# Performance work log

Measured on AMD Instinct MI355X. Metric: run time of the kernel, lower is better.

## Reference

```python
import jax, jax.numpy as jnp
import numpy as np

B, C, HW, N, FS = 8, 1024, 14, 512, 14  # batch, channels, fmap size, num ROIs, feature_scal
SCALE = 1.0 / 16.0
IMG = 224.0


def setup_inputs() -> dict:
    key = jax.random.key(0)
    k1, k2, k3, k4 = jax.random.split(key, 4)
    tensor = jax.random.normal(k1, (B, C, HW, HW), dtype=jnp.float32)
    # ROI rows: [batch_idx, x1, y1, x2, y2] in 224-px image coords, guaranteed x2>x1, y2>y1
    bidx = jax.random.randint(k2, (N,), 0, B).astype(jnp.float32)
    xy1 = jax.random.uniform(k3, (N, 2), minval=0.0, maxval=100.0)
    wh = jax.random.uniform(k4, (N, 2), minval=16.0, maxval=124.0)
    xy2 = jnp.minimum(xy1 + wh, IMG)
    ROI = jnp.concatenate([bidx[:, None], xy1, xy2], axis=1)  # [N,5]
    return {"tensor": tensor, "ROI": ROI}


def _pool_matrix(start, end, fs):
    # Adaptive-avg-pool of slice [start:end] (length L) to fs bins, expressed as a
    # [N, fs(out bins), fs(input positions)] averaging matrix.
    L = end - start  # [N] ints, >= 1
    i = jnp.arange(fs)  # output bins
    b0 = (i[None, :] * L[:, None]) // fs                      # [N,fs] bin start (rel)
    b1 = ((i[None, :] + 1) * L[:, None] + fs - 1) // fs       # [N,fs] bin end (rel, excl)
    pos = jnp.arange(fs)[None, None, :] - start[:, None, None]  # [N,1,fs] rel input pos
    mask = (pos >= b0[:, :, None]) & (pos < b1[:, :, None])     # [N,fs,fs]
    cnt = jnp.maximum(b1 - b0, 1).astype(jnp.float32)
    return mask.astype(jnp.float32) / cnt[:, :, None]


def reference(tensor, ROI):
    fm_no = ROI[:, 0].astype(jnp.int32)          # which batch element per ROI
    coords = ROI[:, 1:] * SCALE                  # [N,4] = x1,y1,x2,y2 in fmap coords
    x1 = jnp.maximum(jnp.floor(coords[:, 0]), 0).astype(jnp.int32)
    y1 = jnp.maximum(jnp.floor(coords[:, 1]), 0).astype(jnp.int32)
    x2 = jnp.minimum(jnp.ceil(coords[:, 2]), FS).astype(jnp.int32)
    y2 = jnp.minimum(jnp.ceil(coords[:, 3]), FS).astype(jnp.int32)
    # torch code slices fm[:, :, x1:x2, y1:y2] -> x indexes rows (H), y indexes cols (W)
    Mr = _pool_matrix(x1, x2, FS)  # [N,14,14] row pooling
    Mc = _pool_matrix(y1, y2, FS)  # [N,14,14] col pooling
    fms = tensor[fm_no]            # [N,C,14,14] gather per-ROI feature map
    # pooled[n,c,i,j] = sum_{h,w} Mr[n,i,h] * fms[n,c,h,w] * Mc[n,j,w]
    return jnp.einsum('nih,nchw,njw->ncij', Mr, fms, Mc)
```

## Files before the change

### kernel.cpp

```cpp
#include <hip/hip_runtime.h>


#define FS_      14
#define PER_CH   196
#define C_       1024
#define CPB      32
#define QPC      49
#define NSTAGE4  (CPB * PER_CH / 4)
#define ACT      245

#if defined(__has_builtin)
# if __has_builtin(__builtin_amdgcn_global_load_lds)
#  define USE_GLL 1
# endif
#endif

__global__ __launch_bounds__(256) void roi_pool_kernel(
    const float* __restrict__ tensor,
    const float* __restrict__ roi,
    float* __restrict__ out)
{
    __shared__ float s_plane[CPB * PER_CH + 4];
    __shared__ alignas(16) int   s_o00[PER_CH], s_o10[PER_CH];
    __shared__ alignas(16) float s_mw[PER_CH], s_mh[PER_CH], s_inv[PER_CH];

    const unsigned bx = blockIdx.x;
    const unsigned n  = bx >> 5;
    const unsigned c0 = (bx & 31u) * CPB;

    const float* r = roi + n * 5;
    const int fm = (int)r[0];
    const int x1 = max((int)floorf(r[1] * 0.0625f), 0);
    const int y1 = max((int)floorf(r[2] * 0.0625f), 0);
    const int x2 = min((int)ceilf(r[3] * 0.0625f), FS_);
    const int y2 = min((int)ceilf(r[4] * 0.0625f), FS_);
    const unsigned Lh = (unsigned)(x2 - x1);
    const unsigned Lw = (unsigned)(y2 - y1);

    const unsigned tid = threadIdx.x;

    if (tid < PER_CH) {
        const unsigned p = tid;
        const unsigned i = p / 14u;
        const unsigned j = p - i * 14u;
        const unsigned h0 = (i * Lh) / 14u;
        const unsigned h1 = ((i + 1u) * Lh + 13u) / 14u;
        const unsigned w0 = (j * Lw) / 14u;
        const unsigned w1 = ((j + 1u) * Lw + 13u) / 14u;
        const int dh = (int)(h1 - h0) - 1;
        const int dw = (int)(w1 - w0) - 1;
        const int a00 = (x1 + (int)h0) * FS_ + (y1 + (int)w0);
        s_o00[p] = a00 * 4;
        s_o10[p] = (a00 + FS_ * dh) * 4;
        s_mw[p]  = (float)dw;
        s_mh[p]  = (float)dh;
        const int cnt = (dh + 1) * (dw + 1);
        s_inv[p] = (cnt == 1) ? 1.0f : ((cnt == 2) ? 0.5f : 0.25f);
    } else if (tid < PER_CH + 4u) {
        s_plane[CPB * PER_CH + (tid - PER_CH)] = 0.0f;
    }

    const float4* __restrict__ src4 =
        (const float4*)(tensor + ((size_t)fm * C_ + c0) * PER_CH);
    float4* __restrict__ dst4 = (float4*)s_plane;
#pragma unroll
    for (unsigned k = 0; k < 7; ++k) {
        unsigned fi = k * 256u + tid;
        if (fi < NSTAGE4) {
#if defined(USE_GLL)
            __builtin_amdgcn_global_load_lds(
                (const __attribute__((address_space(1))) void*)(src4 + fi),
                (__attribute__((address_space(3))) void*)(dst4 + fi),
                16, 0, 0);
#else
            dst4[fi] = src4[fi];
#endif
        }
    }

    __syncthreads();

    if (tid < ACT) {
        const unsigned tc = tid / QPC;
        const unsigned q  = tid - tc * QPC;

        int   O00[4], O10[4];
        float MW[4], MH[4], INV[4];
#pragma unroll
        for (int k = 0; k < 4; ++k) {
            const unsigned p = q + QPC * (unsigned)k;
            O00[k] = s_o00[p];
            O10[k] = s_o10[p];
            MW[k]  = s_mw[p];
            MH[k]  = s_mh[p];
            INV[k] = s_inv[p];
        }

        float* __restrict__ ob =
            out + ((size_t)n * C_ + c0) * PER_CH + q;

#pragma unroll
        for (unsigned it = 0; it < 7; ++it) {
            const unsigned cl = it * 5u + tc;
            if (cl >= CPB) continue;
            const char* pb = (const char*)s_plane + cl * (PER_CH * 4);
            float* __restrict__ op = ob + cl * PER_CH;

#pragma unroll
            for (int k = 0; k < 4; ++k) {
                const char* p0 = pb + O00[k];
                const float v00 = *(const float*)(p0);
                const float v01 = *(const float*)(p0 + 4);
                const char* p1 = pb + O10[k];
                const float v10 = *(const float*)(p1);
                const float v11 = *(const float*)(p1 + 4);
                const float s = fmaf(MW[k], v01, v00) + MH[k] * fmaf(MW[k], v11, v10);
                op[k * QPC] = s * INV[k];
            }
        }
    }
}

extern "C" void kernel_launch(void* const* d_in, const int* in_sizes, int n_in,
                              void* d_out, int out_size, void* d_ws, size_t ws_size,
                              hipStream_t stream) {
    const float* tensor = (const float*)d_in[0];
    const float* roi    = (const float*)d_in[1];
    float* out = (float*)d_out;

    const int blocks = (out_size / (CPB * PER_CH));
    roi_pool_kernel<<<blocks, 256, 0, stream>>>(tensor, roi, out);
}
```

Before: 413.8 us.

## Stage each batch channel group once and loop over matching ROIs

The grid moves from one block per (ROI, channel group) to one block per (batch, channel group, ROI slice). Each block stages the feature planes once into LDS and then loops over the ROIs in its slice that belong to that batch, rebuilding the pooling tables for each one. This reuses LDS-staged data across ROIs and cuts redundant global reads of the input tensor. In exchange it adds two block barriers per ROI, a scan over candidate ROI indices, and fewer blocks (1024 instead of 16384), with per-block work uneven across batches.

After: 420.9 us. Within noise of the previous version (+1.7%).

```diff
diff --git a/kernel.cpp b/kernel.cpp
--- a/kernel.cpp
+++ b/kernel.cpp
@@ -8,6 +8,9 @@
 #define QPC      49
 #define NSTAGE4  (CPB * PER_CH / 4)
 #define ACT      245
+#define NROI     512
+#define NSLICE   4
+#define CAND     (NROI / NSLICE)
 
 #if defined(__has_builtin)
 # if __has_builtin(__builtin_amdgcn_global_load_lds)
@@ -23,45 +26,24 @@
     __shared__ float s_plane[CPB * PER_CH + 4];
     __shared__ alignas(16) int   s_o00[PER_CH], s_o10[PER_CH];
     __shared__ alignas(16) float s_mw[PER_CH], s_mh[PER_CH], s_inv[PER_CH];
+    __shared__ int s_fm[CAND];
 
-    const unsigned bx = blockIdx.x;
-    const unsigned n  = bx >> 5;
-    const unsigned c0 = (bx & 31u) * CPB;
-
-    const float* r = roi + n * 5;
-    const int fm = (int)r[0];
-    const int x1 = max((int)floorf(r[1] * 0.0625f), 0);
-    const int y1 = max((int)floorf(r[2] * 0.0625f), 0);
-    const int x2 = min((int)ceilf(r[3] * 0.0625f), FS_);
-    const int y2 = min((int)ceilf(r[4] * 0.0625f), FS_);
-    const unsigned Lh = (unsigned)(x2 - x1);
-    const unsigned Lw = (unsigned)(y2 - y1);
+    const unsigned bx    = blockIdx.x;
+    const unsigned slice = bx & 3u;
+    const unsigned cg    = (bx >> 2) & 31u;
+    const unsigned b     = bx >> 7;
+    const unsigned c0    = cg * CPB;
 
     const unsigned tid = threadIdx.x;
 
-    if (tid < PER_CH) {
-        const unsigned p = tid;
-        const unsigned i = p / 14u;
-        const unsigned j = p - i * 14u;
-        const unsigned h0 = (i * Lh) / 14u;
-        const unsigned h1 = ((i + 1u) * Lh + 13u) / 14u;
-        const unsigned w0 = (j * Lw) / 14u;
-        const unsigned w1 = ((j + 1u) * Lw + 13u) / 14u;
-        const int dh = (int)(h1 - h0) - 1;
-        const int dw = (int)(w1 - w0) - 1;
-        const int a00 = (x1 + (int)h0) * FS_ + (y1 + (int)w0);
-        s_o00[p] = a00 * 4;
-        s_o10[p] = (a00 + FS_ * dh) * 4;
-        s_mw[p]  = (float)dw;
-        s_mh[p]  = (float)dh;
-        const int cnt = (dh + 1) * (dw + 1);
-        s_inv[p] = (cnt == 1) ? 1.0f : ((cnt == 2) ? 0.5f : 0.25f);
-    } else if (tid < PER_CH + 4u) {
-        s_plane[CPB * PER_CH + (tid - PER_CH)] = 0.0f;
+    if (tid < CAND) {
+        s_fm[tid] = (int)roi[(size_t)(slice + 4u * tid) * 5];
+    } else if (tid < CAND + 4u) {
+        s_plane[CPB * PER_CH + (tid - CAND)] = 0.0f;
     }
 
     const float4* __restrict__ src4 =
-        (const float4*)(tensor + ((size_t)fm * C_ + c0) * PER_CH);
+        (const float4*)(tensor + ((size_t)b * C_ + c0) * PER_CH);
     float4* __restrict__ dst4 = (float4*)s_plane;
 #pragma unroll
     for (unsigned k = 0; k < 7; ++k) {
@@ -80,44 +62,79 @@
 
     __syncthreads();
 
-    if (tid < ACT) {
-        const unsigned tc = tid / QPC;
-        const unsigned q  = tid - tc * QPC;
+    const unsigned tc = tid / QPC;
+    const unsigned q  = tid - tc * QPC;
 
-        int   O00[4], O10[4];
-        float MW[4], MH[4], INV[4];
+    for (unsigned ci = 0; ci < CAND; ++ci) {
+        if (s_fm[ci] != (int)b) continue;
+        const unsigned n = slice + 4u * ci;
+
+        if (tid < PER_CH) {
+            const float* r = roi + (size_t)n * 5;
+            const int x1 = max((int)floorf(r[1] * 0.0625f), 0);
+            const int y1 = max((int)floorf(r[2] * 0.0625f), 0);
+            const int x2 = min((int)ceilf(r[3] * 0.0625f), FS_);
+            const int y2 = min((int)ceilf(r[4] * 0.0625f), FS_);
+            const unsigned Lh = (unsigned)(x2 - x1);
+            const unsigned Lw = (unsigned)(y2 - y1);
+
+            const unsigned p = tid;
+            const unsigned i = p / 14u;
+            const unsigned j = p - i * 14u;
+            const unsigned h0 = (i * Lh) / 14u;
+            const unsigned h1 = ((i + 1u) * Lh + 13u) / 14u;
+            const unsigned w0 = (j * Lw) / 14u;
+            const unsigned w1 = ((j + 1u) * Lw + 13u) / 14u;
+            const int dh = (int)(h1 - h0) - 1;
+            const int dw = (int)(w1 - w0) - 1;
+            const int a00 = (x1 + (int)h0) * FS_ + (y1 + (int)w0);
+            s_o00[p] = a00 * 4;
+            s_o10[p] = (a00 + FS_ * dh) * 4;
+            s_mw[p]  = (float)dw;
+            s_mh[p]  = (float)dh;
+            const int cnt = (dh + 1) * (dw + 1);
+            s_inv[p] = (cnt == 1) ? 1.0f : ((cnt == 2) ? 0.5f : 0.25f);
+        }
+        __syncthreads();
+
+        if (tid < ACT) {
+            int   O00[4], O10[4];
+            float MW[4], MH[4], INV[4];
 #pragma unroll
-        for (int k = 0; k < 4; ++k) {
-            const unsigned p = q + QPC * (unsigned)k;
-            O00[k] = s_o00[p];
-            O10[k] = s_o10[p];
-            MW[k]  = s_mw[p];
-            MH[k]  = s_mh[p];
-            INV[k] = s_inv[p];
-        }
+            for (int k = 0; k < 4; ++k) {
+                const unsigned p = q + QPC * (unsigned)k;
+                O00[k] = s_o00[p];
+                O10[k] = s_o10[p];
+                MW[k]  = s_mw[p];
+                MH[k]  = s_mh[p];
+                INV[k] = s_inv[p];
+            }
 
-        float* __restrict__ ob =
-            out + ((size_t)n * C_ + c0) * PER_CH + q;
+            float* __restrict__ ob =
+                out + ((size_t)n * C_ + c0) * PER_CH + q;
 
 #pragma unroll
-        for (unsigned it = 0; it < 7; ++it) {
-            const unsigned cl = it * 5u + tc;
-            if (cl >= CPB) continue;
-            const char* pb = (const char*)s_plane + cl * (PER_CH * 4);
-            float* __restrict__ op = ob + cl * PER_CH;
+            for (unsigned it = 0; it < 7; ++it) {
+                const unsigned cl = it * 5u + tc;
+                if (cl >= CPB) continue;
+                const char* pb = (const char*)s_plane + cl * (PER_CH * 4);
+                float* __restrict__ op = ob + cl * PER_CH;
 
 #pragma unroll
-            for (int k = 0; k < 4; ++k) {
-                const char* p0 = pb + O00[k];
-                const float v00 = *(const float*)(p0);
-                const float v01 = *(const float*)(p0 + 4);
-                const char* p1 = pb + O10[k];
-                const float v10 = *(const float*)(p1);
-                const float v11 = *(const float*)(p1 + 4);
-                const float s = fmaf(MW[k], v01, v00) + MH[k] * fmaf(MW[k], v11, v10);
-                op[k * QPC] = s * INV[k];
+                for (int k = 0; k < 4; ++k) {
+                    const char* p0 = pb + O00[k];
+                    const float v00 = *(const float*)(p0);
+                    const float v01 = *(const float*)(p0 + 4);
+                    const char* p1 = pb + O10[k];
+                    const float v10 = *(const float*)(p1);
+                    const float v11 = *(const float*)(p1 + 4);
+                    const float s = fmaf(MW[k], v01, v00)
+                                  + MH[k] * fmaf(MW[k], v11, v10);
+                    op[k * QPC] = s * INV[k];
+                }
             }
         }
+        __syncthreads();
     }
 }
 
@@ -128,6 +145,6 @@
     const float* roi    = (const float*)d_in[1];
     float* out = (float*)d_out;
 
-    const int blocks = (out_size / (CPB * PER_CH));
+    const int blocks = 8 * 32 * NSLICE;
     roi_pool_kernel<<<blocks, 256, 0, stream>>>(tensor, roi, out);
 }
```
